# Optimization experiments

Hardware: AMD Instinct MI355X
Metric: run time of the kernel (lower is better)

The kernel has to match this reference:

```python
import jax, jax.numpy as jnp
import numpy as np

N_NODES = 50000
N_EDGES = 600000
N_ELEMENTS = 100
N_RBF = 50
D = 128
CUTOFF = 5.0


def setup_inputs() -> dict:
    key = jax.random.key(0)
    ks = jax.random.split(key, 10)
    node_type = jax.random.randint(ks[0], (N_NODES,), 0, N_ELEMENTS)
    x_nodes = jax.random.normal(ks[1], (N_NODES, D), dtype=jnp.float32)
    src = jax.random.randint(ks[2], (N_EDGES,), 0, N_NODES)
    dst = jax.random.randint(ks[3], (N_EDGES,), 0, N_NODES)
    rbf_edges = jax.random.normal(ks[4], (N_EDGES, N_RBF), dtype=jnp.float32)
    dist = jax.random.uniform(ks[5], (N_EDGES,), dtype=jnp.float32) * (CUTOFF * 1.2)
    emb = jax.random.normal(ks[6], (N_ELEMENTS, D), dtype=jnp.float32) * 0.1
    W_e = jax.random.normal(ks[7], (D, N_RBF), dtype=jnp.float32) * (1.0 / np.sqrt(N_RBF))
    b_e = jnp.zeros((D,), dtype=jnp.float32)
    W_c = jax.random.normal(ks[8], (D, 2 * D), dtype=jnp.float32) * (1.0 / np.sqrt(2 * D))
    b_c = jnp.zeros((D,), dtype=jnp.float32)
    return {"node_type": node_type, "x_nodes": x_nodes, "src": src, "dst": dst,
            "rbf_edges": rbf_edges, "dist": dist, "emb": emb,
            "W_e": W_e, "b_e": b_e, "W_c": W_c, "b_c": b_c}


def cosine_cutoff(dist, cutoff):
    # 0.5*(cos(pi*d/cutoff)+1), zeroed beyond cutoff
    w = 0.5 * (jnp.cos(dist * (jnp.pi / cutoff)) + 1.0)
    return w * (dist < cutoff).astype(dist.dtype)


def reference(node_type, x_nodes, src, dst, rbf_edges, dist, emb, W_e, b_e, W_c, b_c):
    # node embedding from atom type: [N, D]
    x_neighbors = emb[node_type]
    # edge projection weighted by cutoff: [E, D]
    x_edges = (rbf_edges @ W_e.T + b_e) * cosine_cutoff(dist, CUTOFF)[:, None]
    # gather source node embedding, multiply by edge embedding, scatter-sum to dst
    msg = x_neighbors[src] * x_edges  # [E, D]
    x_integrated = jax.ops.segment_sum(msg, dst, num_segments=N_NODES)  # [N, D]
    # concat + combine linear: [N, D]
    x_combine = jnp.concatenate([x_nodes, x_integrated], axis=-1)
    return x_combine @ W_c.T + b_c
```

## Files before the change

### kernel.cpp

```cpp
#include <hip/hip_runtime.h>
#include <hip/hip_bf16.h>

constexpr int NN   = 50000;
constexpr int NE   = 600000;
constexpr int NRBF = 50;
constexpr int DIM  = 128;
constexpr float CUT = 5.0f;
constexpr float PI_F = 3.14159265358979323846f;

constexpr int CAP = 32;

constexpr size_t OFF_DEG   = 0;
constexpr size_t OFF_OVFC  = (size_t)NN * 4;
constexpr size_t OFF_EID   = 200960;
constexpr size_t OFF_CCB   = OFF_EID  + (size_t)NN * CAP * 4;
constexpr size_t OFF_TAUB  = OFF_CCB  + (size_t)NN * CAP * 4;
constexpr size_t OFF_OVF   = OFF_TAUB + (size_t)NN * CAP * 4;
constexpr size_t OFF_WAUG  = OFF_OVF  + (size_t)NE * 4;
constexpr size_t OFF_EPERM = OFF_WAUG + 128 * 64 * 2;
constexpr size_t OFF_XI    = OFF_EPERM + 100 * 128 * 2;


typedef __attribute__((ext_vector_type(4))) float f32x4;
typedef __attribute__((ext_vector_type(8))) short short8;

__device__ __forceinline__ float bf2f(unsigned short u) {
    return __uint_as_float(((unsigned int)u) << 16);
}
__device__ __forceinline__ unsigned short f2bf(float f) {
    return __bfloat16_as_ushort(__float2bfloat16(f));
}

__global__ __launch_bounds__(256)
void bucket_prep(const int* __restrict__ dst, const float* __restrict__ dist,
                 const int* __restrict__ src, const int* __restrict__ node_type,
                 int* __restrict__ deg, int* __restrict__ eid,
                 float* __restrict__ ccb, int* __restrict__ taub,
                 int* __restrict__ ovf, int* __restrict__ ovf_cnt,
                 const float* __restrict__ W_e, const float* __restrict__ b_e,
                 const float* __restrict__ emb,
                 unsigned short* __restrict__ W_aug, unsigned short* __restrict__ emb_perm)
{
    const int e = blockIdx.x * 256 + threadIdx.x;

    if (e < NE) {
        const float dd = dist[e];
        if (dd < CUT) {
            const float w = 0.5f * (__cosf(dd * (PI_F / CUT)) + 1.0f);
            const int n = dst[e];
            const int pos = atomicAdd(&deg[n], 1);
            if (pos < CAP) {
                eid[n * CAP + pos]  = e;
                ccb[n * CAP + pos]  = w;
                taub[n * CAP + pos] = node_type[src[e]];
            } else {
                ovf[atomicAdd(ovf_cnt, 1)] = e;
            }
        }
    }

    if (e < 128 * 64) {
        const int d = e >> 6, k = e & 63;
        float v = 0.0f;
        if (k < NRBF)       v = W_e[d * NRBF + k];
        else if (k == NRBF) v = b_e[d];
        W_aug[e] = f2bf(v);
    } else if (e < 128 * 64 + 100 * 128) {
        const int i = e - 128 * 64;
        const int tau = i >> 7, p = i & 127;
        const int d = 16 * (p & 7) + (p >> 3);
        emb_perm[i] = f2bf(emb[tau * DIM + d]);
    }
}

__global__ __launch_bounds__(256)
void gather_fused(const float* __restrict__ rbf,
                  const int* __restrict__ deg, const int* __restrict__ eid,
                  const float* __restrict__ ccb, const int* __restrict__ taub,
                  const unsigned short* __restrict__ W_aug,
                  const unsigned short* __restrict__ emb_perm,
                  const int* __restrict__ ovf, const int* __restrict__ ovf_cnt,
                  const int* __restrict__ dst, const float* __restrict__ dist,
                  const int* __restrict__ src, const int* __restrict__ node_type,
                  unsigned short* __restrict__ xi)
{
    __shared__ __align__(16) unsigned short wlds[128 * 72];
    __shared__ int   eid_s[256];
    __shared__ float ccb_s[256];
    __shared__ int   taub_s[256];
    __shared__ int   deg_s[8];

    const int t = threadIdx.x, l = t & 63;
    const int wv = t >> 6;
    const int c = l & 15, g = l >> 4;
    const int n0 = blockIdx.x * 8;

    {
        const int node_t = n0 + (t >> 5);
        if (node_t < NN) {
            const int gi = n0 * CAP + t;
            eid_s[t]  = eid[gi];
            ccb_s[t]  = ccb[gi];
            taub_s[t] = taub[gi];
        }
        if (t < 8) deg_s[t] = (n0 + t < NN) ? deg[n0 + t] : 0;
        #pragma unroll
        for (int i = 0; i < 4; ++i) {
            const int ch = i * 256 + t;
            const int row = ch >> 3, f = ch & 7;
            *(int4*)((char*)wlds + row * 144 + f * 16) = ((const int4*)W_aug)[ch];
        }
    }
    __syncthreads();

    #pragma unroll
    for (int ni = 0; ni < 2; ++ni) {
        const int nl = wv * 2 + ni;
        const int n  = n0 + nl;
        if (n >= NN) continue;

        const int dn   = deg_s[nl];
        const int degn = dn < CAP ? dn : CAP;
        const int mb   = nl * 32;

        float v[8] = {};

        for (int j0 = 0; j0 < degn; j0 += 16) {
            const int slot = j0 + c;
            int   ea  = 0;
            float ccl = 0.0f;
            if (slot < degn) {
                ea  = eid_s[mb + slot];
                ccl = ccb_s[mb + slot];
            }
            const float* rp = rbf + (size_t)ea * NRBF;

            const float2* rp2 = (const float2*)rp;
            const float2 r0 = rp2[4 * g];
            const float2 r1 = rp2[4 * g + 1];
            const float2 r2 = rp2[4 * g + 2];
            const float2 r3 = rp2[4 * g + 3];
            float2 q0 = make_float2(0.f, 0.f), q1 = q0, q2 = q0, q3 = q0;
            if (g < 2) {
                q0 = rp2[16 + 4 * g];
                q1 = rp2[17 + 4 * g];
                q2 = rp2[18 + 4 * g];
                q3 = rp2[19 + 4 * g];
            } else if (g == 2) {
                q0 = rp2[24];
            }

            short8 a0, a1;
            a0[0] = (short)f2bf(ccl * r0.x); a0[1] = (short)f2bf(ccl * r0.y);
            a0[2] = (short)f2bf(ccl * r1.x); a0[3] = (short)f2bf(ccl * r1.y);
            a0[4] = (short)f2bf(ccl * r2.x); a0[5] = (short)f2bf(ccl * r2.y);
            a0[6] = (short)f2bf(ccl * r3.x); a0[7] = (short)f2bf(ccl * r3.y);
            a1[0] = (short)f2bf(ccl * q0.x); a1[1] = (short)f2bf(ccl * q0.y);
            a1[2] = (short)f2bf(ccl * q1.x); a1[3] = (short)f2bf(ccl * q1.y);
            a1[4] = (short)f2bf(ccl * q2.x); a1[5] = (short)f2bf(ccl * q2.y);
            a1[6] = (short)f2bf(ccl * q3.x); a1[7] = (short)f2bf(ccl * q3.y);
            if (g == 2) {
                a1[2] = (short)f2bf(ccl);
                a1[3] = 0; a1[4] = 0; a1[5] = 0; a1[6] = 0; a1[7] = 0;
            }

            f32x4 acc[8] = {};
            #pragma unroll
            for (int nt = 0; nt < 8; ++nt) {
                const short8 bf0 =
                    *(const short8*)((const char*)wlds + (nt * 16 + c) * 144 + g * 16);
                acc[nt] = __builtin_amdgcn_mfma_f32_16x16x32_bf16(a0, bf0, acc[nt], 0, 0, 0);
            }
            #pragma unroll
            for (int nt = 0; nt < 8; ++nt) {
                const short8 bf1 =
                    *(const short8*)((const char*)wlds + (nt * 16 + c) * 144 + (4 + g) * 16);
                acc[nt] = __builtin_amdgcn_mfma_f32_16x16x32_bf16(a1, bf1, acc[nt], 0, 0, 0);
            }

            #pragma unroll
            for (int r = 0; r < 4; ++r) {
                const int jr = j0 + 4 * g + r;
                if (jr < degn) {
                    const int rw = taub_s[mb + jr];
                    const int4 em = *(const int4*)(emb_perm + rw * DIM + 8 * c);
                    const unsigned int* ep = (const unsigned int*)&em;
                    #pragma unroll
                    for (int q = 0; q < 4; ++q) {
                        const float m0 = bf2f((unsigned short)(ep[q] & 0xffff));
                        const float m1 = bf2f((unsigned short)(ep[q] >> 16));
                        v[2 * q]     += bf2f(f2bf(acc[2 * q][r]     * m0));
                        v[2 * q + 1] += bf2f(f2bf(acc[2 * q + 1][r] * m1));
                    }
                }
            }
        }

        const int ocnt = ovf_cnt[0];
        for (int j = 0; j < ocnt; ++j) {
            const int e = ovf[j];
            if (dst[e] != n) continue;
            const float dd  = dist[e];
            const float ccl = 0.5f * (__cosf(dd * (PI_F / CUT)) + 1.0f);
            if (g == 0) {
                const int tau = node_type[src[e]];
                const float* rp = rbf + (size_t)e * NRBF;
                const float ccb16 = bf2f(f2bf(ccl));
                #pragma unroll
                for (int q = 0; q < 8; ++q) {
                    const int d = 16 * q + c;
                    float s = bf2f(W_aug[d * 64 + NRBF]) * ccb16;
                    for (int k = 0; k < NRBF; ++k)
                        s += bf2f(W_aug[d * 64 + k]) * bf2f(f2bf(ccl * rp[k]));
                    v[q] += bf2f(f2bf(s * bf2f(emb_perm[tau * DIM + 8 * c + q])));
                }
            }
        }

        #pragma unroll
        for (int q = 0; q < 8; ++q) {
            v[q] += __shfl_xor(v[q], 16);
            v[q] += __shfl_xor(v[q], 32);
        }

        float s0 = v[0], s1 = v[1];
        if (g == 1)      { s0 = v[2]; s1 = v[3]; }
        else if (g == 2) { s0 = v[4]; s1 = v[5]; }
        else if (g == 3) { s0 = v[6]; s1 = v[7]; }
        xi[(size_t)n * DIM + 32 * g + c]      = f2bf(s0);
        xi[(size_t)n * DIM + 32 * g + 16 + c] = f2bf(s1);
    }
}

__global__ __launch_bounds__(256)
void combine_mfma(const float* __restrict__ x_nodes, const __hip_bfloat16* __restrict__ xi,
                  const float* __restrict__ W_c, const float* __restrict__ b_c,
                  float* __restrict__ out)
{
    __shared__ unsigned short As[64][72];
    __shared__ unsigned short Bs[128][72];

    const int t  = threadIdx.x;
    const int wv = t >> 6;
    const int l  = t & 63;
    const int n0 = blockIdx.x * 64;

    f32x4 acc[8] = {};

    for (int kc = 0; kc < 4; ++kc) {
        const int kb = kc * 64;
        if (kc) __syncthreads();
        {
            const int r  = t >> 2;
            const int c0 = (t & 3) * 16;
            const int n  = n0 + r;
            if (kc < 2) {
                float4 v[4];
                if (n < NN) {
                    const float4* p = (const float4*)(x_nodes + (size_t)n * DIM + kb + c0);
                    v[0] = p[0]; v[1] = p[1]; v[2] = p[2]; v[3] = p[3];
                } else {
                    v[0] = v[1] = v[2] = v[3] = make_float4(0.f, 0.f, 0.f, 0.f);
                }
                unsigned short* dp = &As[r][c0];
                #pragma unroll
                for (int q = 0; q < 4; ++q) {
                    *(ushort2*)&dp[q * 4]     = make_ushort2(f2bf(v[q].x), f2bf(v[q].y));
                    *(ushort2*)&dp[q * 4 + 2] = make_ushort2(f2bf(v[q].z), f2bf(v[q].w));
                }
            } else {
                int4 v0 = make_int4(0, 0, 0, 0), v1 = make_int4(0, 0, 0, 0);
                if (n < NN) {
                    const int4* p = (const int4*)(xi + (size_t)n * DIM + (kb - DIM) + c0);
                    v0 = p[0];
                    v1 = p[1];
                }
                *(int4*)&As[r][c0]     = v0;
                *(int4*)&As[r][c0 + 8] = v1;
            }
        }
        {
            const int dch = t >> 1;
            const int c0  = (t & 1) * 32;
            const float4* p = (const float4*)(W_c + (size_t)dch * (2 * DIM) + kb + c0);
            unsigned short* dp = &Bs[dch][c0];
            #pragma unroll
            for (int q = 0; q < 8; ++q) {
                const float4 v = p[q];
                *(ushort2*)&dp[q * 4]     = make_ushort2(f2bf(v.x), f2bf(v.y));
                *(ushort2*)&dp[q * 4 + 2] = make_ushort2(f2bf(v.z), f2bf(v.w));
            }
        }
        __syncthreads();
        #pragma unroll
        for (int s = 0; s < 2; ++s) {
            const int ko = s * 32 + (l >> 4) * 8;
            const short8 af = *(const short8*)&As[wv * 16 + (l & 15)][ko];
            #pragma unroll
            for (int nt = 0; nt < 8; ++nt) {
                const short8 bf = *(const short8*)&Bs[nt * 16 + (l & 15)][ko];
                acc[nt] = __builtin_amdgcn_mfma_f32_16x16x32_bf16(af, bf, acc[nt], 0, 0, 0);
            }
        }
    }

    const int col = l & 15;
    const int rq  = (l >> 4) * 4;
    #pragma unroll
    for (int nt = 0; nt < 8; ++nt) {
        const int dim = nt * 16 + col;
        const float bc = b_c[dim];
        #pragma unroll
        for (int r = 0; r < 4; ++r) {
            const int node = n0 + wv * 16 + rq + r;
            if (node < NN)
                out[(size_t)node * DIM + dim] = acc[nt][r] + bc;
        }
    }
}

extern "C" void kernel_launch(void* const* d_in, const int* in_sizes, int n_in,
                              void* d_out, int out_size, void* d_ws, size_t ws_size,
                              hipStream_t stream)
{
    const int*   node_type = (const int*)  d_in[0];
    const float* x_nodes   = (const float*)d_in[1];
    const int*   src       = (const int*)  d_in[2];
    const int*   dst       = (const int*)  d_in[3];
    const float* rbf       = (const float*)d_in[4];
    const float* dist      = (const float*)d_in[5];
    const float* emb       = (const float*)d_in[6];
    const float* W_e       = (const float*)d_in[7];
    const float* b_e       = (const float*)d_in[8];
    const float* W_c       = (const float*)d_in[9];
    const float* b_c       = (const float*)d_in[10];
    float* out = (float*)d_out;

    char* ws = (char*)d_ws;
    int*            deg      = (int*)(ws + OFF_DEG);
    int*            ovf_cnt  = (int*)(ws + OFF_OVFC);
    int*            eid      = (int*)(ws + OFF_EID);
    float*          ccb      = (float*)(ws + OFF_CCB);
    int*            taub     = (int*)(ws + OFF_TAUB);
    int*            ovf      = (int*)(ws + OFF_OVF);
    unsigned short* W_aug    = (unsigned short*)(ws + OFF_WAUG);
    unsigned short* emb_perm = (unsigned short*)(ws + OFF_EPERM);
    unsigned short* xi       = (unsigned short*)(ws + OFF_XI);

    hipMemsetAsync(deg, 0, (NN + 1) * sizeof(int), stream);

    bucket_prep<<<(NE + 255) / 256, 256, 0, stream>>>(
        dst, dist, src, node_type, deg, eid, ccb, taub, ovf, ovf_cnt,
        W_e, b_e, emb, W_aug, emb_perm);

    gather_fused<<<(NN + 7) / 8, 256, 0, stream>>>(
        rbf, deg, eid, ccb, taub, W_aug, emb_perm,
        ovf, ovf_cnt, dst, dist, src, node_type, xi);

    combine_mfma<<<(NN + 63) / 64, 256, 0, stream>>>(
        x_nodes, (const __hip_bfloat16*)xi, W_c, b_c, out);
}
```

Baseline: 367.3 us.

## Pack edge bucket into int4 and software-pipeline rbf loads across nodes

```diff
diff --git a/kernel.cpp b/kernel.cpp
--- a/kernel.cpp
+++ b/kernel.cpp
@@ -12,10 +12,8 @@
 
 constexpr size_t OFF_DEG   = 0;
 constexpr size_t OFF_OVFC  = (size_t)NN * 4;
-constexpr size_t OFF_EID   = 200960;
-constexpr size_t OFF_CCB   = OFF_EID  + (size_t)NN * CAP * 4;
-constexpr size_t OFF_TAUB  = OFF_CCB  + (size_t)NN * CAP * 4;
-constexpr size_t OFF_OVF   = OFF_TAUB + (size_t)NN * CAP * 4;
+constexpr size_t OFF_EBUF  = 200960;
+constexpr size_t OFF_OVF   = OFF_EBUF + (size_t)NN * CAP * 16;
 constexpr size_t OFF_WAUG  = OFF_OVF  + (size_t)NE * 4;
 constexpr size_t OFF_EPERM = OFF_WAUG + 128 * 64 * 2;
 constexpr size_t OFF_XI    = OFF_EPERM + 100 * 128 * 2;
@@ -34,8 +32,7 @@
 __global__ __launch_bounds__(256)
 void bucket_prep(const int* __restrict__ dst, const float* __restrict__ dist,
                  const int* __restrict__ src, const int* __restrict__ node_type,
-                 int* __restrict__ deg, int* __restrict__ eid,
-                 float* __restrict__ ccb, int* __restrict__ taub,
+                 int* __restrict__ deg, int4* __restrict__ ebuf,
                  int* __restrict__ ovf, int* __restrict__ ovf_cnt,
                  const float* __restrict__ W_e, const float* __restrict__ b_e,
                  const float* __restrict__ emb,
@@ -50,9 +47,8 @@
             const int n = dst[e];
             const int pos = atomicAdd(&deg[n], 1);
             if (pos < CAP) {
-                eid[n * CAP + pos]  = e;
-                ccb[n * CAP + pos]  = w;
-                taub[n * CAP + pos] = node_type[src[e]];
+                ebuf[(size_t)n * CAP + pos] =
+                    make_int4(e, __float_as_int(w), node_type[src[e]], 0);
             } else {
                 ovf[atomicAdd(ovf_cnt, 1)] = e;
             }
@@ -73,10 +69,168 @@
     }
 }
 
-__global__ __launch_bounds__(256)
+struct NodeLoad {
+    float2 r0, r1, r2, r3, q0, q1, q2, q3;
+    float  ccl;
+    int    degn;
+    int    mb;
+};
+
+__device__ __forceinline__ void issue_node(const int4* __restrict__ eb_s,
+                                           const int* __restrict__ deg_s,
+                                           const float* __restrict__ rbf,
+                                           int nl, int c, int g, NodeLoad& L)
+{
+    const int dn = deg_s[nl];
+    L.degn = dn < CAP ? dn : CAP;
+    L.mb   = nl * 32;
+    int ea = 0; L.ccl = 0.0f;
+    if (c < L.degn) {
+        const int4 eb = eb_s[L.mb + c];
+        ea    = eb.x;
+        L.ccl = __int_as_float(eb.y);
+    }
+    const float2* rp2 = (const float2*)(rbf + (size_t)ea * NRBF);
+    L.r0 = rp2[4 * g];     L.r1 = rp2[4 * g + 1];
+    L.r2 = rp2[4 * g + 2]; L.r3 = rp2[4 * g + 3];
+    L.q0 = make_float2(0.f, 0.f); L.q1 = L.q0; L.q2 = L.q0; L.q3 = L.q0;
+    if (g < 2) {
+        L.q0 = rp2[16 + 4 * g]; L.q1 = rp2[17 + 4 * g];
+        L.q2 = rp2[18 + 4 * g]; L.q3 = rp2[19 + 4 * g];
+    } else if (g == 2) {
+        L.q0 = rp2[24];
+    }
+}
+
+__device__ __forceinline__ void round_compute(
+    float ccl, float2 r0, float2 r1, float2 r2, float2 r3,
+    float2 q0, float2 q1, float2 q2, float2 q3,
+    int j0, int degn, int mb, int c, int g,
+    const unsigned short* __restrict__ wlds, const int4* __restrict__ eb_s,
+    const unsigned short* __restrict__ emb_perm, float v[8])
+{
+    short8 a0, a1;
+    a0[0] = (short)f2bf(ccl * r0.x); a0[1] = (short)f2bf(ccl * r0.y);
+    a0[2] = (short)f2bf(ccl * r1.x); a0[3] = (short)f2bf(ccl * r1.y);
+    a0[4] = (short)f2bf(ccl * r2.x); a0[5] = (short)f2bf(ccl * r2.y);
+    a0[6] = (short)f2bf(ccl * r3.x); a0[7] = (short)f2bf(ccl * r3.y);
+    a1[0] = (short)f2bf(ccl * q0.x); a1[1] = (short)f2bf(ccl * q0.y);
+    a1[2] = (short)f2bf(ccl * q1.x); a1[3] = (short)f2bf(ccl * q1.y);
+    a1[4] = (short)f2bf(ccl * q2.x); a1[5] = (short)f2bf(ccl * q2.y);
+    a1[6] = (short)f2bf(ccl * q3.x); a1[7] = (short)f2bf(ccl * q3.y);
+    if (g == 2) {
+        a1[2] = (short)f2bf(ccl);
+        a1[3] = 0; a1[4] = 0; a1[5] = 0; a1[6] = 0; a1[7] = 0;
+    }
+
+    f32x4 acc[8] = {};
+    #pragma unroll
+    for (int nt = 0; nt < 8; ++nt) {
+        const short8 bf0 = *(const short8*)((const char*)wlds + (nt * 16 + c) * 144 + g * 16);
+        acc[nt] = __builtin_amdgcn_mfma_f32_16x16x32_bf16(a0, bf0, acc[nt], 0, 0, 0);
+    }
+    #pragma unroll
+    for (int nt = 0; nt < 8; ++nt) {
+        const short8 bf1 = *(const short8*)((const char*)wlds + (nt * 16 + c) * 144 + (4 + g) * 16);
+        acc[nt] = __builtin_amdgcn_mfma_f32_16x16x32_bf16(a1, bf1, acc[nt], 0, 0, 0);
+    }
+
+    #pragma unroll
+    for (int r = 0; r < 4; ++r) {
+        const int jr = j0 + 4 * g + r;
+        if (jr < degn) {
+            const int rw = eb_s[mb + jr].z;
+            const int4 em = *(const int4*)(emb_perm + rw * DIM + 8 * c);
+            const unsigned int* ep = (const unsigned int*)&em;
+            #pragma unroll
+            for (int q = 0; q < 4; ++q) {
+                const float m0 = bf2f((unsigned short)(ep[q] & 0xffff));
+                const float m1 = bf2f((unsigned short)(ep[q] >> 16));
+                v[2 * q]     += bf2f(f2bf(acc[2 * q][r]     * m0));
+                v[2 * q + 1] += bf2f(f2bf(acc[2 * q + 1][r] * m1));
+            }
+        }
+    }
+}
+
+__device__ __forceinline__ void compute_node(
+    const NodeLoad& L, int c, int g,
+    const unsigned short* __restrict__ wlds, const int4* __restrict__ eb_s,
+    const unsigned short* __restrict__ emb_perm, const float* __restrict__ rbf,
+    float v[8])
+{
+    round_compute(L.ccl, L.r0, L.r1, L.r2, L.r3, L.q0, L.q1, L.q2, L.q3,
+                  0, L.degn, L.mb, c, g, wlds, eb_s, emb_perm, v);
+    if (L.degn > 16) {
+        int ea = 0; float ccl = 0.0f;
+        const int slot = 16 + c;
+        if (slot < L.degn) {
+            const int4 eb = eb_s[L.mb + slot];
+            ea  = eb.x;
+            ccl = __int_as_float(eb.y);
+        }
+        const float2* rp2 = (const float2*)(rbf + (size_t)ea * NRBF);
+        const float2 r0 = rp2[4 * g],     r1 = rp2[4 * g + 1];
+        const float2 r2 = rp2[4 * g + 2], r3 = rp2[4 * g + 3];
+        float2 q0 = make_float2(0.f, 0.f), q1 = q0, q2 = q0, q3 = q0;
+        if (g < 2) {
+            q0 = rp2[16 + 4 * g]; q1 = rp2[17 + 4 * g];
+            q2 = rp2[18 + 4 * g]; q3 = rp2[19 + 4 * g];
+        } else if (g == 2) {
+            q0 = rp2[24];
+        }
+        round_compute(ccl, r0, r1, r2, r3, q0, q1, q2, q3,
+                      16, L.degn, L.mb, c, g, wlds, eb_s, emb_perm, v);
+    }
+}
+
+__device__ __forceinline__ void finish_node(
+    float v[8], int n, int c, int g, int ocnt,
+    const int* __restrict__ ovf, const int* __restrict__ dst,
+    const float* __restrict__ dist, const int* __restrict__ src,
+    const int* __restrict__ node_type, const float* __restrict__ rbf,
+    const unsigned short* __restrict__ W_aug_g,
+    const unsigned short* __restrict__ emb_perm, unsigned short* __restrict__ xi)
+{
+    for (int j = 0; j < ocnt; ++j) {
+        const int e = ovf[j];
+        if (dst[e] != n) continue;
+        const float dd  = dist[e];
+        const float ccl = 0.5f * (__cosf(dd * (PI_F / CUT)) + 1.0f);
+        if (g == 0) {
+            const int tau = node_type[src[e]];
+            const float* rp = rbf + (size_t)e * NRBF;
+            const float ccb16 = bf2f(f2bf(ccl));
+            #pragma unroll
+            for (int q = 0; q < 8; ++q) {
+                const int d = 16 * q + c;
+                float s = bf2f(W_aug_g[d * 64 + NRBF]) * ccb16;
+                for (int k = 0; k < NRBF; ++k)
+                    s += bf2f(W_aug_g[d * 64 + k]) * bf2f(f2bf(ccl * rp[k]));
+                v[q] += bf2f(f2bf(s * bf2f(emb_perm[tau * DIM + 8 * c + q])));
+            }
+        }
+    }
+
+    #pragma unroll
+    for (int q = 0; q < 8; ++q) {
+        v[q] += __shfl_xor(v[q], 16);
+        v[q] += __shfl_xor(v[q], 32);
+    }
+
+    float s0 = v[0], s1 = v[1];
+    if (g == 1)      { s0 = v[2]; s1 = v[3]; }
+    else if (g == 2) { s0 = v[4]; s1 = v[5]; }
+    else if (g == 3) { s0 = v[6]; s1 = v[7]; }
+    if (n < NN) {
+        xi[(size_t)n * DIM + 32 * g + c]      = f2bf(s0);
+        xi[(size_t)n * DIM + 32 * g + 16 + c] = f2bf(s1);
+    }
+}
+
+__global__ __launch_bounds__(256, 4)
 void gather_fused(const float* __restrict__ rbf,
-                  const int* __restrict__ deg, const int* __restrict__ eid,
-                  const float* __restrict__ ccb, const int* __restrict__ taub,
+                  const int* __restrict__ deg, const int4* __restrict__ ebuf,
                   const unsigned short* __restrict__ W_aug,
                   const unsigned short* __restrict__ emb_perm,
                   const int* __restrict__ ovf, const int* __restrict__ ovf_cnt,
@@ -85,25 +239,22 @@
                   unsigned short* __restrict__ xi)
 {
     __shared__ __align__(16) unsigned short wlds[128 * 72];
-    __shared__ int   eid_s[256];
-    __shared__ float ccb_s[256];
-    __shared__ int   taub_s[256];
-    __shared__ int   deg_s[8];
+    __shared__ int4 eb_s[16 * 32];
+    __shared__ int  deg_s[16];
 
     const int t = threadIdx.x, l = t & 63;
     const int wv = t >> 6;
     const int c = l & 15, g = l >> 4;
-    const int n0 = blockIdx.x * 8;
+    const int n0 = blockIdx.x * 16;
 
     {
-        const int node_t = n0 + (t >> 5);
-        if (node_t < NN) {
-            const int gi = n0 * CAP + t;
-            eid_s[t]  = eid[gi];
-            ccb_s[t]  = ccb[gi];
-            taub_s[t] = taub[gi];
-        }
-        if (t < 8) deg_s[t] = (n0 + t < NN) ? deg[n0 + t] : 0;
+        #pragma unroll
+        for (int i = 0; i < 2; ++i) {
+            const int s = i * 256 + t;
+            const int node = n0 + (s >> 5);
+            eb_s[s] = (node < NN) ? ebuf[(size_t)n0 * CAP + s] : make_int4(0, 0, 0, 0);
+        }
+        if (t < 16) deg_s[t] = (n0 + t < NN) ? deg[n0 + t] : 0;
         #pragma unroll
         for (int i = 0; i < 4; ++i) {
             const int ch = i * 256 + t;
@@ -112,123 +263,39 @@
         }
     }
     __syncthreads();
-
-    #pragma unroll
-    for (int ni = 0; ni < 2; ++ni) {
-        const int nl = wv * 2 + ni;
-        const int n  = n0 + nl;
-        if (n >= NN) continue;
-
-        const int dn   = deg_s[nl];
-        const int degn = dn < CAP ? dn : CAP;
-        const int mb   = nl * 32;
-
+    const int ocnt = ovf_cnt[0];
+
+    const int nbase = wv * 4;
+
+    NodeLoad L0, L1;
+    issue_node(eb_s, deg_s, rbf, nbase + 0, c, g, L0);
+    issue_node(eb_s, deg_s, rbf, nbase + 1, c, g, L1);
+
+    {
         float v[8] = {};
-
-        for (int j0 = 0; j0 < degn; j0 += 16) {
-            const int slot = j0 + c;
-            int   ea  = 0;
-            float ccl = 0.0f;
-            if (slot < degn) {
-                ea  = eid_s[mb + slot];
-                ccl = ccb_s[mb + slot];
-            }
-            const float* rp = rbf + (size_t)ea * NRBF;
-
-            const float2* rp2 = (const float2*)rp;
-            const float2 r0 = rp2[4 * g];
-            const float2 r1 = rp2[4 * g + 1];
-            const float2 r2 = rp2[4 * g + 2];
-            const float2 r3 = rp2[4 * g + 3];
-            float2 q0 = make_float2(0.f, 0.f), q1 = q0, q2 = q0, q3 = q0;
-            if (g < 2) {
-                q0 = rp2[16 + 4 * g];
-                q1 = rp2[17 + 4 * g];
-                q2 = rp2[18 + 4 * g];
-                q3 = rp2[19 + 4 * g];
-            } else if (g == 2) {
-                q0 = rp2[24];
-            }
-
-            short8 a0, a1;
-            a0[0] = (short)f2bf(ccl * r0.x); a0[1] = (short)f2bf(ccl * r0.y);
-            a0[2] = (short)f2bf(ccl * r1.x); a0[3] = (short)f2bf(ccl * r1.y);
-            a0[4] = (short)f2bf(ccl * r2.x); a0[5] = (short)f2bf(ccl * r2.y);
-            a0[6] = (short)f2bf(ccl * r3.x); a0[7] = (short)f2bf(ccl * r3.y);
-            a1[0] = (short)f2bf(ccl * q0.x); a1[1] = (short)f2bf(ccl * q0.y);
-            a1[2] = (short)f2bf(ccl * q1.x); a1[3] = (short)f2bf(ccl * q1.y);
-            a1[4] = (short)f2bf(ccl * q2.x); a1[5] = (short)f2bf(ccl * q2.y);
-            a1[6] = (short)f2bf(ccl * q3.x); a1[7] = (short)f2bf(ccl * q3.y);
-            if (g == 2) {
-                a1[2] = (short)f2bf(ccl);
-                a1[3] = 0; a1[4] = 0; a1[5] = 0; a1[6] = 0; a1[7] = 0;
-            }
-
-            f32x4 acc[8] = {};
-            #pragma unroll
-            for (int nt = 0; nt < 8; ++nt) {
-                const short8 bf0 =
-                    *(const short8*)((const char*)wlds + (nt * 16 + c) * 144 + g * 16);
-                acc[nt] = __builtin_amdgcn_mfma_f32_16x16x32_bf16(a0, bf0, acc[nt], 0, 0, 0);
-            }
-            #pragma unroll
-            for (int nt = 0; nt < 8; ++nt) {
-                const short8 bf1 =
-                    *(const short8*)((const char*)wlds + (nt * 16 + c) * 144 + (4 + g) * 16);
-                acc[nt] = __builtin_amdgcn_mfma_f32_16x16x32_bf16(a1, bf1, acc[nt], 0, 0, 0);
-            }
-
-            #pragma unroll
-            for (int r = 0; r < 4; ++r) {
-                const int jr = j0 + 4 * g + r;
-                if (jr < degn) {
-                    const int rw = taub_s[mb + jr];
-                    const int4 em = *(const int4*)(emb_perm + rw * DIM + 8 * c);
-                    const unsigned int* ep = (const unsigned int*)&em;
-                    #pragma unroll
-                    for (int q = 0; q < 4; ++q) {
-                        const float m0 = bf2f((unsigned short)(ep[q] & 0xffff));
-                        const float m1 = bf2f((unsigned short)(ep[q] >> 16));
-                        v[2 * q]     += bf2f(f2bf(acc[2 * q][r]     * m0));
-                        v[2 * q + 1] += bf2f(f2bf(acc[2 * q + 1][r] * m1));
-                    }
-                }
-            }
-        }
-
-        const int ocnt = ovf_cnt[0];
-        for (int j = 0; j < ocnt; ++j) {
-            const int e = ovf[j];
-            if (dst[e] != n) continue;
-            const float dd  = dist[e];
-            const float ccl = 0.5f * (__cosf(dd * (PI_F / CUT)) + 1.0f);
-            if (g == 0) {
-                const int tau = node_type[src[e]];
-                const float* rp = rbf + (size_t)e * NRBF;
-                const float ccb16 = bf2f(f2bf(ccl));
-                #pragma unroll
-                for (int q = 0; q < 8; ++q) {
-                    const int d = 16 * q + c;
-                    float s = bf2f(W_aug[d * 64 + NRBF]) * ccb16;
-                    for (int k = 0; k < NRBF; ++k)
-                        s += bf2f(W_aug[d * 64 + k]) * bf2f(f2bf(ccl * rp[k]));
-                    v[q] += bf2f(f2bf(s * bf2f(emb_perm[tau * DIM + 8 * c + q])));
-                }
-            }
-        }
-
-        #pragma unroll
-        for (int q = 0; q < 8; ++q) {
-            v[q] += __shfl_xor(v[q], 16);
-            v[q] += __shfl_xor(v[q], 32);
-        }
-
-        float s0 = v[0], s1 = v[1];
-        if (g == 1)      { s0 = v[2]; s1 = v[3]; }
-        else if (g == 2) { s0 = v[4]; s1 = v[5]; }
-        else if (g == 3) { s0 = v[6]; s1 = v[7]; }
-        xi[(size_t)n * DIM + 32 * g + c]      = f2bf(s0);
-        xi[(size_t)n * DIM + 32 * g + 16 + c] = f2bf(s1);
+        compute_node(L0, c, g, wlds, eb_s, emb_perm, rbf, v);
+        issue_node(eb_s, deg_s, rbf, nbase + 2, c, g, L0);
+        finish_node(v, n0 + nbase + 0, c, g, ocnt, ovf, dst, dist, src,
+                    node_type, rbf, W_aug, emb_perm, xi);
+    }
+    {
+        float v[8] = {};
+        compute_node(L1, c, g, wlds, eb_s, emb_perm, rbf, v);
+        issue_node(eb_s, deg_s, rbf, nbase + 3, c, g, L1);
+        finish_node(v, n0 + nbase + 1, c, g, ocnt, ovf, dst, dist, src,
+                    node_type, rbf, W_aug, emb_perm, xi);
+    }
+    {
+        float v[8] = {};
+        compute_node(L0, c, g, wlds, eb_s, emb_perm, rbf, v);
+        finish_node(v, n0 + nbase + 2, c, g, ocnt, ovf, dst, dist, src,
+                    node_type, rbf, W_aug, emb_perm, xi);
+    }
+    {
+        float v[8] = {};
+        compute_node(L1, c, g, wlds, eb_s, emb_perm, rbf, v);
+        finish_node(v, n0 + nbase + 3, c, g, ocnt, ovf, dst, dist, src,
+                    node_type, rbf, W_aug, emb_perm, xi);
     }
 }
 
@@ -339,9 +406,7 @@
     char* ws = (char*)d_ws;
     int*            deg      = (int*)(ws + OFF_DEG);
     int*            ovf_cnt  = (int*)(ws + OFF_OVFC);
-    int*            eid      = (int*)(ws + OFF_EID);
-    float*          ccb      = (float*)(ws + OFF_CCB);
-    int*            taub     = (int*)(ws + OFF_TAUB);
+    int4*           ebuf     = (int4*)(ws + OFF_EBUF);
     int*            ovf      = (int*)(ws + OFF_OVF);
     unsigned short* W_aug    = (unsigned short*)(ws + OFF_WAUG);
     unsigned short* emb_perm = (unsigned short*)(ws + OFF_EPERM);
@@ -350,11 +415,11 @@
     hipMemsetAsync(deg, 0, (NN + 1) * sizeof(int), stream);
 
     bucket_prep<<<(NE + 255) / 256, 256, 0, stream>>>(
-        dst, dist, src, node_type, deg, eid, ccb, taub, ovf, ovf_cnt,
+        dst, dist, src, node_type, deg, ebuf, ovf, ovf_cnt,
         W_e, b_e, emb, W_aug, emb_perm);
 
-    gather_fused<<<(NN + 7) / 8, 256, 0, stream>>>(
-        rbf, deg, eid, ccb, taub, W_aug, emb_perm,
+    gather_fused<<<(NN + 15) / 16, 256, 0, stream>>>(
+        rbf, deg, ebuf, W_aug, emb_perm,
         ovf, ovf_cnt, dst, dist, src, node_type, xi);
 
     combine_mfma<<<(NN + 63) / 64, 256, 0, stream>>>(
```

Result: slower. 466.7 us (+27.1%).
